# Performance work log

Measured on AMD Instinct MI355X. Metric: run time of the kernel, lower is better.

The kernel has to match this reference:

```python
import jax, jax.numpy as jnp
import numpy as np

FEATURE_SIZE = 40960
FIRST_HIDDEN = 512
HALF = FIRST_HIDDEN // 2  # 256, per-perspective width
SECOND_HIDDEN = 32
BATCH = 4096


def setup_inputs() -> dict:
    key = jax.random.key(0)
    ks = jax.random.split(key, 10)
    inp = {
        "white_features": jax.random.uniform(ks[0], (BATCH, FEATURE_SIZE), dtype=jnp.float32),
        "black_features": jax.random.uniform(ks[1], (BATCH, FEATURE_SIZE), dtype=jnp.float32),
        # input_layer1 and input_layer2 share weight_float/bias_float -> single param
        "w_in": jax.random.normal(ks[2], (HALF, FEATURE_SIZE), dtype=jnp.float32) * 0.1,
        "b_in": jnp.zeros((HALF,), dtype=jnp.float32),
        "w_h1": jax.random.normal(ks[3], (SECOND_HIDDEN, FIRST_HIDDEN), dtype=jnp.float32) * 0.1,
        "b_h1": jnp.zeros((SECOND_HIDDEN,), dtype=jnp.float32),
        "w_h2": jax.random.normal(ks[4], (SECOND_HIDDEN, SECOND_HIDDEN), dtype=jnp.float32) * 0.1,
        "b_h2": jnp.zeros((SECOND_HIDDEN,), dtype=jnp.float32),
        "w_out": jax.random.normal(ks[5], (1, SECOND_HIDDEN), dtype=jnp.float32) * 0.1,
        "b_out": jnp.zeros((1,), dtype=jnp.float32),
    }
    return inp


def _clipped_relu(x):
    return jnp.clip(x, 0.0, 1.0)


def reference(white_features, black_features, w_in, b_in, w_h1, b_h1, w_h2, b_h2, w_out, b_out):
    # Perspective feature transform (shared weights), training-mode float path
    out1 = white_features @ w_in.T + b_in  # [B, 256]
    out2 = black_features @ w_in.T + b_in  # [B, 256]
    x = _clipped_relu(jnp.concatenate([out1, out2], axis=1))  # [B, 512]
    x = _clipped_relu(x @ w_h1.T + b_h1)  # [B, 32]
    x = _clipped_relu(x @ w_h2.T + b_h2)  # [B, 32]
    return x @ w_out.T + b_out  # [B, 1]
```

## Files before the change

### kernel.cpp

```cpp
#include <hip/hip_runtime.h>
#include <hip/hip_fp16.h>


#define FEAT 40960
#define PSTRIDE (8192ull * 256ull)
#define KSPLIT 8
#define KCHUNK (FEAT / KSPLIT)
#define NSTEP 160
#define WTILE_BYTES 16384
#define WWS_BYTES (1280ull * WTILE_BYTES)

using floatx4 = __attribute__((ext_vector_type(4))) float;
using half8   = __attribute__((ext_vector_type(8))) _Float16;

__global__ __launch_bounds__(256) void nnue_wprep(
    const float* __restrict__ w_in, _Float16* __restrict__ Wws)
{
    const int bid = blockIdx.x;
    const int T   = (bid & 7) * NSTEP + (bid >> 3);
    char* base = (char*)Wws + (size_t)T * WTILE_BYTES;
    const int tid = threadIdx.x;
    const int kg0 = T * 32;
#pragma unroll
    for (int i = 0; i < 4; ++i) {
        const int G = tid + i * 256;
        const int r = G >> 2, g = G & 3;
        const float* src = w_in + (size_t)r * FEAT + kg0 + g * 8;
        floatx4 v0 = *reinterpret_cast<const floatx4*>(src);
        floatx4 v1 = *reinterpret_cast<const floatx4*>(src + 4);
        half8 h;
#pragma unroll
        for (int j = 0; j < 4; ++j) { h[j] = (_Float16)v0[j]; h[4 + j] = (_Float16)v1[j]; }
        *reinterpret_cast<half8*>(base + r * 64 + ((g ^ ((r >> 1) & 3)) << 4)) = h;
    }
}

template <typename PT>
__global__ __launch_bounds__(512, 4) void nnue_gemm_v9(
    const float* __restrict__ white, const float* __restrict__ black,
    const _Float16* __restrict__ Wws, PT* __restrict__ P)
{
    __shared__ __align__(16) _Float16 Ws[3][256 * 32];

    const int tid  = threadIdx.x;
    const int lane = tid & 63;
    const int wave = tid >> 6;

    const int ks = blockIdx.x & 7;
    const int mb = blockIdx.x >> 3;

    const float* Abase = (mb < 32)
        ? (white + (size_t)mb * 128 * FEAT)
        : (black + (size_t)(mb - 32) * 128 * FEAT);
    const int k0 = ks * KCHUNK;

    const int frow = lane & 15;
    const int fhi  = lane >> 4;

    const float* Aptr = Abase + (size_t)(wave * 16 + frow) * FEAT + fhi * 8 + k0;

    const int kb = (fhi * 16) ^ (((frow >> 1) & 3) << 4);

    const char* wsrc0 = (const char*)Wws + (size_t)(ks * NSTEP) * WTILE_BYTES
                        + wave * 2048 + lane * 16;

    floatx4 acc[16];
    const floatx4 zero = {0.f, 0.f, 0.f, 0.f};
#pragma unroll
    for (int n = 0; n < 16; ++n) acc[n] = zero;

    floatx4 raA0, raA1, raB0, raB1;

    auto issueW = [&](int t, int wb) {
        const char* g = wsrc0 + (size_t)t * WTILE_BYTES;
        char* l = (char*)&Ws[wb][0] + wave * 2048;
        __builtin_amdgcn_global_load_lds(
            (const __attribute__((address_space(1))) unsigned int*)g,
            (__attribute__((address_space(3))) unsigned int*)l, 16, 0, 0);
        __builtin_amdgcn_global_load_lds(
            (const __attribute__((address_space(1))) unsigned int*)(g + 1024),
            (__attribute__((address_space(3))) unsigned int*)(l + 1024), 16, 0, 0);
    };

    auto cvt = [&](const floatx4& a0, const floatx4& a1) {
        half8 h;
#pragma unroll
        for (int j = 0; j < 4; ++j) { h[j] = (_Float16)a0[j]; h[4 + j] = (_Float16)a1[j]; }
        return h;
    };

    auto mfmaStep = [&](int wb, half8 af) {
        const char* wbase = (const char*)&Ws[wb][0];
#pragma unroll
        for (int n = 0; n < 16; ++n) {
            half8 bf = *reinterpret_cast<const half8*>(
                wbase + (n * 16 + frow) * 64 + kb);
            acc[n] = __builtin_amdgcn_mfma_f32_16x16x32_f16(af, bf, acc[n], 0, 0, 0);
        }
    };

    auto stepf = [&](int t, int wbW, int wbR,
                     floatx4& c0, floatx4& c1, floatx4& n0, floatx4& n1) {
        issueW(t + 2, wbW);
        __builtin_amdgcn_sched_barrier(0);
        n0 = *reinterpret_cast<const floatx4*>(Aptr + (size_t)(t + 1) * 32);
        n1 = *reinterpret_cast<const floatx4*>(Aptr + (size_t)(t + 1) * 32 + 4);
        half8 af = cvt(c0, c1);
        mfmaStep(wbR, af);
        asm volatile("s_waitcnt vmcnt(4) lgkmcnt(0)" ::: "memory");
        __builtin_amdgcn_s_barrier();
        __builtin_amdgcn_sched_barrier(0);
    };

    issueW(0, 0);
    issueW(1, 1);
    __builtin_amdgcn_sched_barrier(0);
    raA0 = *reinterpret_cast<const floatx4*>(Aptr);
    raA1 = *reinterpret_cast<const floatx4*>(Aptr + 4);
    asm volatile("s_waitcnt vmcnt(4)" ::: "memory");
    __builtin_amdgcn_s_barrier();
    __builtin_amdgcn_sched_barrier(0);

    for (int tb = 0; tb < 156; tb += 6) {
        stepf(tb + 0, 2, 0, raA0, raA1, raB0, raB1);
        stepf(tb + 1, 0, 1, raB0, raB1, raA0, raA1);
        stepf(tb + 2, 1, 2, raA0, raA1, raB0, raB1);
        stepf(tb + 3, 2, 0, raB0, raB1, raA0, raA1);
        stepf(tb + 4, 0, 1, raA0, raA1, raB0, raB1);
        stepf(tb + 5, 1, 2, raB0, raB1, raA0, raA1);
    }
    stepf(156, 2, 0, raA0, raA1, raB0, raB1);
    stepf(157, 0, 1, raB0, raB1, raA0, raA1);
    raB0 = *reinterpret_cast<const floatx4*>(Aptr + (size_t)159 * 32);
    raB1 = *reinterpret_cast<const floatx4*>(Aptr + (size_t)159 * 32 + 4);
    {
        half8 af = cvt(raA0, raA1);
        mfmaStep(2, af);
    }
    asm volatile("s_waitcnt vmcnt(4) lgkmcnt(0)" ::: "memory");
    __builtin_amdgcn_s_barrier();
    __builtin_amdgcn_sched_barrier(0);
    {
        half8 af = cvt(raB0, raB1);
        mfmaStep(0, af);
    }

    PT* Pb = P + (size_t)ks * PSTRIDE + (size_t)mb * 128 * 256;
#pragma unroll
    for (int n = 0; n < 16; ++n)
#pragma unroll
        for (int r = 0; r < 4; ++r) {
            const int row = wave * 16 + fhi * 4 + r;
            const int col = n * 16 + frow;
            Pb[(size_t)row * 256 + col] = (PT)acc[n][r];
        }
}

template <typename PT>
__global__ __launch_bounds__(256) void nnue_tail(
    const PT* __restrict__ P,
    const float* __restrict__ b_in,
    const float* __restrict__ w_h1, const float* __restrict__ b_h1,
    const float* __restrict__ w_h2, const float* __restrict__ b_h2,
    const float* __restrict__ w_out, const float* __restrict__ b_out,
    float* __restrict__ out)
{
    __shared__ float xs[32][512];
    __shared__ float w1[32][513];
    __shared__ float w2[32][33];
    __shared__ float h1[32][33];
    __shared__ float h2[32][33];
    __shared__ float wo[32];

    const int tid = threadIdx.x;
    const int b0  = blockIdx.x * 32;

    for (int i = tid; i < 32 * 512; i += 256) w1[i >> 9][i & 511] = w_h1[i];
    for (int i = tid; i < 32 * 32; i += 256)  w2[i >> 5][i & 31]  = w_h2[i];
    if (tid < 32) wo[tid] = w_out[tid];

    for (int i = tid; i < 32 * 512; i += 256) {
        const int r = i >> 9, c = i & 511;
        const int persp = c >> 8, n = c & 255;
        const size_t prow = (size_t)(b0 + r) + (persp ? 4096u : 0u);
        float v = 0.f;
#pragma unroll
        for (int s = 0; s < KSPLIT; ++s)
            v += (float)P[(size_t)s * PSTRIDE + prow * 256 + n];
        v += b_in[n];
        xs[r][c] = fminf(fmaxf(v, 0.f), 1.f);
    }
    __syncthreads();

    for (int p = tid; p < 32 * 32; p += 256) {
        const int o = p & 31, r = p >> 5;
        float a = b_h1[o];
        for (int j = 0; j < 512; ++j) a += xs[r][j] * w1[o][j];
        h1[r][o] = fminf(fmaxf(a, 0.f), 1.f);
    }
    __syncthreads();

    for (int p = tid; p < 32 * 32; p += 256) {
        const int o = p & 31, r = p >> 5;
        float a = b_h2[o];
        for (int j = 0; j < 32; ++j) a += h1[r][j] * w2[o][j];
        h2[r][o] = fminf(fmaxf(a, 0.f), 1.f);
    }
    __syncthreads();

    if (tid < 32) {
        float a = b_out[0];
        for (int j = 0; j < 32; ++j) a += h2[tid][j] * wo[j];
        out[b0 + tid] = a;
    }
}

__global__ __launch_bounds__(256) void nnue_naive(
    const float* __restrict__ white, const float* __restrict__ black,
    const float* __restrict__ w_in, const float* __restrict__ b_in,
    const float* __restrict__ w_h1, const float* __restrict__ b_h1,
    const float* __restrict__ w_h2, const float* __restrict__ b_h2,
    const float* __restrict__ w_out, const float* __restrict__ b_out,
    float* __restrict__ out)
{
    __shared__ float feat[4096];
    __shared__ float xs[512];
    __shared__ float h1s[32];
    __shared__ float h2s[32];
    const int b = blockIdx.x, tid = threadIdx.x;
    float acc0 = 0.f, acc1 = 0.f;
    for (int c = 0; c < FEAT; c += 2048) {
        for (int i = tid; i < 2048; i += 256) {
            feat[i]        = white[(size_t)b * FEAT + c + i];
            feat[2048 + i] = black[(size_t)b * FEAT + c + i];
        }
        __syncthreads();
        const float* wr = w_in + (size_t)tid * FEAT + c;
        for (int k = 0; k < 2048; ++k) {
            const float w = wr[k];
            acc0 += feat[k] * w;
            acc1 += feat[2048 + k] * w;
        }
        __syncthreads();
    }
    xs[tid]       = fminf(fmaxf(acc0 + b_in[tid], 0.f), 1.f);
    xs[256 + tid] = fminf(fmaxf(acc1 + b_in[tid], 0.f), 1.f);
    __syncthreads();
    if (tid < 32) {
        float a = b_h1[tid];
        for (int j = 0; j < 512; ++j) a += xs[j] * w_h1[tid * 512 + j];
        h1s[tid] = fminf(fmaxf(a, 0.f), 1.f);
    }
    __syncthreads();
    if (tid < 32) {
        float a = b_h2[tid];
        for (int j = 0; j < 32; ++j) a += h1s[j] * w_h2[tid * 32 + j];
        h2s[tid] = fminf(fmaxf(a, 0.f), 1.f);
    }
    __syncthreads();
    if (tid == 0) {
        float a = b_out[0];
        for (int j = 0; j < 32; ++j) a += h2s[j] * w_out[j];
        out[b] = a;
    }
}

extern "C" void kernel_launch(void* const* d_in, const int* in_sizes, int n_in,
                              void* d_out, int out_size, void* d_ws, size_t ws_size,
                              hipStream_t stream)
{
    const float* white = (const float*)d_in[0];
    const float* black = (const float*)d_in[1];
    const float* w_in  = (const float*)d_in[2];
    const float* b_in  = (const float*)d_in[3];
    const float* w_h1  = (const float*)d_in[4];
    const float* b_h1  = (const float*)d_in[5];
    const float* w_h2  = (const float*)d_in[6];
    const float* b_h2  = (const float*)d_in[7];
    const float* w_out = (const float*)d_in[8];
    const float* b_out = (const float*)d_in[9];
    float* out = (float*)d_out;

    const size_t pF32 = KSPLIT * PSTRIDE * sizeof(float);
    const size_t pF16 = KSPLIT * PSTRIDE * sizeof(_Float16);

    if (ws_size >= pF32 + WWS_BYTES) {
        float* P = (float*)d_ws;
        _Float16* Wws = (_Float16*)((char*)d_ws + pF32);
        nnue_wprep<<<dim3(1280), 256, 0, stream>>>(w_in, Wws);
        nnue_gemm_v9<float><<<dim3(512), 512, 0, stream>>>(white, black, Wws, P);
        nnue_tail<float><<<dim3(128), 256, 0, stream>>>(P, b_in, w_h1, b_h1,
                                                        w_h2, b_h2, w_out, b_out, out);
    } else if (ws_size >= pF16 + WWS_BYTES) {
        _Float16* P = (_Float16*)d_ws;
        _Float16* Wws = (_Float16*)((char*)d_ws + pF16);
        nnue_wprep<<<dim3(1280), 256, 0, stream>>>(w_in, Wws);
        nnue_gemm_v9<_Float16><<<dim3(512), 512, 0, stream>>>(white, black, Wws, P);
        nnue_tail<_Float16><<<dim3(128), 256, 0, stream>>>(P, b_in, w_h1, b_h1,
                                                           w_h2, b_h2, w_out, b_out, out);
    } else {
        nnue_naive<<<4096, 256, 0, stream>>>(white, black, w_in, b_in, w_h1, b_h1,
                                             w_h2, b_h2, w_out, b_out, out);
    }
}
```

Measured before the change: 393.9 us.

## Process two K-steps per barrier with four LDS weight buffers

New measurement: 390.4 us. About the same (-0.9%).

```diff
diff --git a/kernel.cpp b/kernel.cpp
--- a/kernel.cpp
+++ b/kernel.cpp
@@ -36,11 +36,11 @@
 }
 
 template <typename PT>
-__global__ __launch_bounds__(512, 4) void nnue_gemm_v9(
+__global__ __launch_bounds__(512, 4) void nnue_gemm_v10(
     const float* __restrict__ white, const float* __restrict__ black,
     const _Float16* __restrict__ Wws, PT* __restrict__ P)
 {
-    __shared__ __align__(16) _Float16 Ws[3][256 * 32];
+    __shared__ __align__(16) _Float16 Ws[4][256 * 32];
 
     const int tid  = threadIdx.x;
     const int lane = tid & 63;
@@ -69,7 +69,7 @@
 #pragma unroll
     for (int n = 0; n < 16; ++n) acc[n] = zero;
 
-    floatx4 raA0, raA1, raB0, raB1;
+    floatx4 cA0, cA1, cA2, cA3, nA0, nA1, nA2, nA3;
 
     auto issueW = [&](int t, int wb) {
         const char* g = wsrc0 + (size_t)t * WTILE_BYTES;
@@ -99,14 +99,20 @@
         }
     };
 
-    auto stepf = [&](int t, int wbW, int wbR,
-                     floatx4& c0, floatx4& c1, floatx4& n0, floatx4& n1) {
-        issueW(t + 2, wbW);
+    auto groupf = [&](int g,
+                      floatx4& c0, floatx4& c1, floatx4& c2, floatx4& c3,
+                      floatx4& n0, floatx4& n1, floatx4& n2, floatx4& n3,
+                      int rb0, int rb1, int wb0, int wb1) {
+        const int t0 = 2 * g;
+        issueW(t0 + 2, wb0);
+        issueW(t0 + 3, wb1);
         __builtin_amdgcn_sched_barrier(0);
-        n0 = *reinterpret_cast<const floatx4*>(Aptr + (size_t)(t + 1) * 32);
-        n1 = *reinterpret_cast<const floatx4*>(Aptr + (size_t)(t + 1) * 32 + 4);
-        half8 af = cvt(c0, c1);
-        mfmaStep(wbR, af);
+        n0 = *reinterpret_cast<const floatx4*>(Aptr + (size_t)(t0 + 2) * 32);
+        n1 = *reinterpret_cast<const floatx4*>(Aptr + (size_t)(t0 + 2) * 32 + 4);
+        n2 = *reinterpret_cast<const floatx4*>(Aptr + (size_t)(t0 + 3) * 32);
+        n3 = *reinterpret_cast<const floatx4*>(Aptr + (size_t)(t0 + 3) * 32 + 4);
+        mfmaStep(rb0, cvt(c0, c1));
+        mfmaStep(rb1, cvt(c2, c3));
         asm volatile("s_waitcnt vmcnt(4) lgkmcnt(0)" ::: "memory");
         __builtin_amdgcn_s_barrier();
         __builtin_amdgcn_sched_barrier(0);
@@ -115,35 +121,21 @@
     issueW(0, 0);
     issueW(1, 1);
     __builtin_amdgcn_sched_barrier(0);
-    raA0 = *reinterpret_cast<const floatx4*>(Aptr);
-    raA1 = *reinterpret_cast<const floatx4*>(Aptr + 4);
+    cA0 = *reinterpret_cast<const floatx4*>(Aptr);
+    cA1 = *reinterpret_cast<const floatx4*>(Aptr + 4);
+    cA2 = *reinterpret_cast<const floatx4*>(Aptr + 32);
+    cA3 = *reinterpret_cast<const floatx4*>(Aptr + 32 + 4);
     asm volatile("s_waitcnt vmcnt(4)" ::: "memory");
     __builtin_amdgcn_s_barrier();
     __builtin_amdgcn_sched_barrier(0);
 
-    for (int tb = 0; tb < 156; tb += 6) {
-        stepf(tb + 0, 2, 0, raA0, raA1, raB0, raB1);
-        stepf(tb + 1, 0, 1, raB0, raB1, raA0, raA1);
-        stepf(tb + 2, 1, 2, raA0, raA1, raB0, raB1);
-        stepf(tb + 3, 2, 0, raB0, raB1, raA0, raA1);
-        stepf(tb + 4, 0, 1, raA0, raA1, raB0, raB1);
-        stepf(tb + 5, 1, 2, raB0, raB1, raA0, raA1);
-    }
-    stepf(156, 2, 0, raA0, raA1, raB0, raB1);
-    stepf(157, 0, 1, raB0, raB1, raA0, raA1);
-    raB0 = *reinterpret_cast<const floatx4*>(Aptr + (size_t)159 * 32);
-    raB1 = *reinterpret_cast<const floatx4*>(Aptr + (size_t)159 * 32 + 4);
-    {
-        half8 af = cvt(raA0, raA1);
-        mfmaStep(2, af);
-    }
-    asm volatile("s_waitcnt vmcnt(4) lgkmcnt(0)" ::: "memory");
-    __builtin_amdgcn_s_barrier();
-    __builtin_amdgcn_sched_barrier(0);
-    {
-        half8 af = cvt(raB0, raB1);
-        mfmaStep(0, af);
-    }
+    for (int p = 0; p < 39; ++p) {
+        groupf(2 * p,     cA0, cA1, cA2, cA3, nA0, nA1, nA2, nA3, 0, 1, 2, 3);
+        groupf(2 * p + 1, nA0, nA1, nA2, nA3, cA0, cA1, cA2, cA3, 2, 3, 0, 1);
+    }
+    groupf(78, cA0, cA1, cA2, cA3, nA0, nA1, nA2, nA3, 0, 1, 2, 3);
+    mfmaStep(2, cvt(nA0, nA1));
+    mfmaStep(3, cvt(nA2, nA3));
 
     PT* Pb = P + (size_t)ks * PSTRIDE + (size_t)mb * 128 * 256;
 #pragma unroll
@@ -288,14 +280,14 @@
         float* P = (float*)d_ws;
         _Float16* Wws = (_Float16*)((char*)d_ws + pF32);
         nnue_wprep<<<dim3(1280), 256, 0, stream>>>(w_in, Wws);
-        nnue_gemm_v9<float><<<dim3(512), 512, 0, stream>>>(white, black, Wws, P);
+        nnue_gemm_v10<float><<<dim3(512), 512, 0, stream>>>(white, black, Wws, P);
         nnue_tail<float><<<dim3(128), 256, 0, stream>>>(P, b_in, w_h1, b_h1,
                                                         w_h2, b_h2, w_out, b_out, out);
     } else if (ws_size >= pF16 + WWS_BYTES) {
         _Float16* P = (_Float16*)d_ws;
         _Float16* Wws = (_Float16*)((char*)d_ws + pF16);
         nnue_wprep<<<dim3(1280), 256, 0, stream>>>(w_in, Wws);
-        nnue_gemm_v9<_Float16><<<dim3(512), 512, 0, stream>>>(white, black, Wws, P);
+        nnue_gemm_v10<_Float16><<<dim3(512), 512, 0, stream>>>(white, black, Wws, P);
         nnue_tail<_Float16><<<dim3(128), 256, 0, stream>>>(P, b_in, w_h1, b_h1,
                                                            w_h2, b_h2, w_out, b_out, out);
     } else {
```

## Fuse first-layer GEMM with MLP tail, dropping split-K partial buffer

Applied to the files above, without the earlier changes.

After: 902.5 us. 129% more time.

```diff
diff --git a/kernel.cpp b/kernel.cpp
--- a/kernel.cpp
+++ b/kernel.cpp
@@ -3,12 +3,9 @@
 
 
 #define FEAT 40960
-#define PSTRIDE (8192ull * 256ull)
-#define KSPLIT 8
-#define KCHUNK (FEAT / KSPLIT)
-#define NSTEP 160
+#define NSTEP 1280
 #define WTILE_BYTES 16384
-#define WWS_BYTES (1280ull * WTILE_BYTES)
+#define WWS_BYTES ((size_t)NSTEP * WTILE_BYTES)
 
 using floatx4 = __attribute__((ext_vector_type(4))) float;
 using half8   = __attribute__((ext_vector_type(8))) _Float16;
@@ -16,8 +13,7 @@
 __global__ __launch_bounds__(256) void nnue_wprep(
     const float* __restrict__ w_in, _Float16* __restrict__ Wws)
 {
-    const int bid = blockIdx.x;
-    const int T   = (bid & 7) * NSTEP + (bid >> 3);
+    const int T = blockIdx.x;
     char* base = (char*)Wws + (size_t)T * WTILE_BYTES;
     const int tid = threadIdx.x;
     const int kg0 = T * 32;
@@ -35,45 +31,50 @@
     }
 }
 
-template <typename PT>
-__global__ __launch_bounds__(512, 4) void nnue_gemm_v9(
+__global__ __launch_bounds__(512, 2) void nnue_fused(
     const float* __restrict__ white, const float* __restrict__ black,
-    const _Float16* __restrict__ Wws, PT* __restrict__ P)
-{
-    __shared__ __align__(16) _Float16 Ws[3][256 * 32];
+    const _Float16* __restrict__ Wws,
+    const float* __restrict__ b_in,
+    const float* __restrict__ w_h1, const float* __restrict__ b_h1,
+    const float* __restrict__ w_h2, const float* __restrict__ b_h2,
+    const float* __restrict__ w_out, const float* __restrict__ b_out,
+    float* __restrict__ out)
+{
+    __shared__ __align__(16) _Float16 Ws[8][256 * 32];
+    __shared__ _Float16 xs[16][520];
+    __shared__ float h1s[16][33];
+    __shared__ float h2s[16][33];
 
     const int tid  = threadIdx.x;
     const int lane = tid & 63;
     const int wave = tid >> 6;
-
-    const int ks = blockIdx.x & 7;
-    const int mb = blockIdx.x >> 3;
-
-    const float* Abase = (mb < 32)
-        ? (white + (size_t)mb * 128 * FEAT)
-        : (black + (size_t)(mb - 32) * 128 * FEAT);
-    const int k0 = ks * KCHUNK;
+    const int ws   = wave >> 2;
+    const int wn   = wave & 3;
+
+    const int b0 = blockIdx.x * 16;
 
     const int frow = lane & 15;
     const int fhi  = lane >> 4;
 
-    const float* Aptr = Abase + (size_t)(wave * 16 + frow) * FEAT + fhi * 8 + k0;
+    const float* Abase = (ws ? black : white) + (size_t)(b0 + frow) * FEAT + fhi * 8;
 
     const int kb = (fhi * 16) ^ (((frow >> 1) & 3) << 4);
 
-    const char* wsrc0 = (const char*)Wws + (size_t)(ks * NSTEP) * WTILE_BYTES
-                        + wave * 2048 + lane * 16;
-
-    floatx4 acc[16];
+    const char* wsrc0 = (const char*)Wws + wave * 2048 + lane * 16;
+
+    const int t0 = (blockIdx.x * 5) % 128;
+    auto wrap = [](int x) { return (x >= NSTEP) ? x - NSTEP : x; };
+
+    floatx4 acc[4];
     const floatx4 zero = {0.f, 0.f, 0.f, 0.f};
 #pragma unroll
-    for (int n = 0; n < 16; ++n) acc[n] = zero;
-
-    floatx4 raA0, raA1, raB0, raB1;
-
-    auto issueW = [&](int t, int wb) {
+    for (int n = 0; n < 4; ++n) acc[n] = zero;
+
+    floatx4 cA[8], nA[8];
+
+    auto issueW = [&](int t, int buf) {
         const char* g = wsrc0 + (size_t)t * WTILE_BYTES;
-        char* l = (char*)&Ws[wb][0] + wave * 2048;
+        char* l = (char*)&Ws[buf][0] + wave * 2048;
         __builtin_amdgcn_global_load_lds(
             (const __attribute__((address_space(1))) unsigned int*)g,
             (__attribute__((address_space(3))) unsigned int*)l, 16, 0, 0);
@@ -82,6 +83,21 @@
             (__attribute__((address_space(3))) unsigned int*)(l + 1024), 16, 0, 0);
     };
 
+    auto issueW4 = [&](int p0, int p1, int p2, int p3, int bb) {
+        issueW(p0, bb); issueW(p1, bb + 1); issueW(p2, bb + 2); issueW(p3, bb + 3);
+    };
+
+    auto loadA4 = [&](floatx4 (&ra)[8], int p0, int p1, int p2, int p3) {
+        ra[0] = *reinterpret_cast<const floatx4*>(Abase + (size_t)p0 * 32);
+        ra[1] = *reinterpret_cast<const floatx4*>(Abase + (size_t)p0 * 32 + 4);
+        ra[2] = *reinterpret_cast<const floatx4*>(Abase + (size_t)p1 * 32);
+        ra[3] = *reinterpret_cast<const floatx4*>(Abase + (size_t)p1 * 32 + 4);
+        ra[4] = *reinterpret_cast<const floatx4*>(Abase + (size_t)p2 * 32);
+        ra[5] = *reinterpret_cast<const floatx4*>(Abase + (size_t)p2 * 32 + 4);
+        ra[6] = *reinterpret_cast<const floatx4*>(Abase + (size_t)p3 * 32);
+        ra[7] = *reinterpret_cast<const floatx4*>(Abase + (size_t)p3 * 32 + 4);
+    };
+
     auto cvt = [&](const floatx4& a0, const floatx4& a1) {
         half8 h;
 #pragma unroll
@@ -89,128 +105,90 @@
         return h;
     };
 
-    auto mfmaStep = [&](int wb, half8 af) {
-        const char* wbase = (const char*)&Ws[wb][0];
-#pragma unroll
-        for (int n = 0; n < 16; ++n) {
-            half8 bf = *reinterpret_cast<const half8*>(
-                wbase + (n * 16 + frow) * 64 + kb);
-            acc[n] = __builtin_amdgcn_mfma_f32_16x16x32_f16(af, bf, acc[n], 0, 0, 0);
-        }
-    };
-
-    auto stepf = [&](int t, int wbW, int wbR,
-                     floatx4& c0, floatx4& c1, floatx4& n0, floatx4& n1) {
-        issueW(t + 2, wbW);
-        __builtin_amdgcn_sched_barrier(0);
-        n0 = *reinterpret_cast<const floatx4*>(Aptr + (size_t)(t + 1) * 32);
-        n1 = *reinterpret_cast<const floatx4*>(Aptr + (size_t)(t + 1) * 32 + 4);
-        half8 af = cvt(c0, c1);
-        mfmaStep(wbR, af);
-        asm volatile("s_waitcnt vmcnt(4) lgkmcnt(0)" ::: "memory");
+    auto mfma4 = [&](int bb, floatx4 (&ra)[8]) {
+#pragma unroll
+        for (int s = 0; s < 4; ++s) {
+            half8 af = cvt(ra[2 * s], ra[2 * s + 1]);
+            const char* wbase = (const char*)&Ws[bb + s][0];
+#pragma unroll
+            for (int n = 0; n < 4; ++n) {
+                const int r = wn * 64 + n * 16 + frow;
+                half8 bf = *reinterpret_cast<const half8*>(wbase + r * 64 + kb);
+                acc[n] = __builtin_amdgcn_mfma_f32_16x16x32_f16(af, bf, acc[n], 0, 0, 0);
+            }
+        }
+    };
+
+    auto grp = [&](int p0, int p1, int p2, int p3,
+                   floatx4 (&cc)[8], floatx4 (&nn)[8], int rb, int wb) {
+        issueW4(p0, p1, p2, p3, wb);
+        __builtin_amdgcn_sched_barrier(0);
+        loadA4(nn, p0, p1, p2, p3);
+        mfma4(rb, cc);
+        asm volatile("s_waitcnt vmcnt(8) lgkmcnt(0)" ::: "memory");
         __builtin_amdgcn_s_barrier();
         __builtin_amdgcn_sched_barrier(0);
     };
 
-    issueW(0, 0);
-    issueW(1, 1);
-    __builtin_amdgcn_sched_barrier(0);
-    raA0 = *reinterpret_cast<const floatx4*>(Aptr);
-    raA1 = *reinterpret_cast<const floatx4*>(Aptr + 4);
-    asm volatile("s_waitcnt vmcnt(4)" ::: "memory");
+    {
+        const int p0 = t0, p1 = wrap(t0 + 1), p2 = wrap(t0 + 2), p3 = wrap(t0 + 3);
+        issueW4(p0, p1, p2, p3, 0);
+        __builtin_amdgcn_sched_barrier(0);
+        loadA4(cA, p0, p1, p2, p3);
+        asm volatile("s_waitcnt vmcnt(8)" ::: "memory");
+        __builtin_amdgcn_s_barrier();
+        __builtin_amdgcn_sched_barrier(0);
+    }
+
+    for (int p = 0; p < 159; ++p) {
+        const int i0 = 8 * p;
+        grp(wrap(t0 + i0 + 4), wrap(t0 + i0 + 5), wrap(t0 + i0 + 6), wrap(t0 + i0 + 7),
+            cA, nA, 0, 4);
+        grp(wrap(t0 + i0 + 8), wrap(t0 + i0 + 9), wrap(t0 + i0 + 10), wrap(t0 + i0 + 11),
+            nA, cA, 4, 0);
+    }
+    grp(wrap(t0 + 1276), wrap(t0 + 1277), wrap(t0 + 1278), wrap(t0 + 1279),
+        cA, nA, 0, 4);
+    mfma4(4, nA);
+    asm volatile("s_waitcnt vmcnt(0) lgkmcnt(0)" ::: "memory");
     __builtin_amdgcn_s_barrier();
     __builtin_amdgcn_sched_barrier(0);
 
-    for (int tb = 0; tb < 156; tb += 6) {
-        stepf(tb + 0, 2, 0, raA0, raA1, raB0, raB1);
-        stepf(tb + 1, 0, 1, raB0, raB1, raA0, raA1);
-        stepf(tb + 2, 1, 2, raA0, raA1, raB0, raB1);
-        stepf(tb + 3, 2, 0, raB0, raB1, raA0, raA1);
-        stepf(tb + 4, 0, 1, raA0, raA1, raB0, raB1);
-        stepf(tb + 5, 1, 2, raB0, raB1, raA0, raA1);
-    }
-    stepf(156, 2, 0, raA0, raA1, raB0, raB1);
-    stepf(157, 0, 1, raB0, raB1, raA0, raA1);
-    raB0 = *reinterpret_cast<const floatx4*>(Aptr + (size_t)159 * 32);
-    raB1 = *reinterpret_cast<const floatx4*>(Aptr + (size_t)159 * 32 + 4);
+#pragma unroll
+    for (int n = 0; n < 4; ++n) {
+        const int bcol = wn * 64 + n * 16 + frow;
+        const float bi = b_in[bcol];
+#pragma unroll
+        for (int r = 0; r < 4; ++r) {
+            const int row = fhi * 4 + r;
+            xs[row][ws * 256 + bcol] = (_Float16)fminf(fmaxf(acc[n][r] + bi, 0.f), 1.f);
+        }
+    }
+    __syncthreads();
+
     {
-        half8 af = cvt(raA0, raA1);
-        mfmaStep(2, af);
-    }
-    asm volatile("s_waitcnt vmcnt(4) lgkmcnt(0)" ::: "memory");
-    __builtin_amdgcn_s_barrier();
-    __builtin_amdgcn_sched_barrier(0);
+        const int r = tid >> 5, o = tid & 31;
+        float a = b_h1[o];
+        const float* wrow = w_h1 + o * 512;
+#pragma unroll 8
+        for (int j = 0; j < 512; ++j) a += (float)xs[r][j] * wrow[j];
+        h1s[r][o] = fminf(fmaxf(a, 0.f), 1.f);
+    }
+    __syncthreads();
+
     {
-        half8 af = cvt(raB0, raB1);
-        mfmaStep(0, af);
-    }
-
-    PT* Pb = P + (size_t)ks * PSTRIDE + (size_t)mb * 128 * 256;
-#pragma unroll
-    for (int n = 0; n < 16; ++n)
-#pragma unroll
-        for (int r = 0; r < 4; ++r) {
-            const int row = wave * 16 + fhi * 4 + r;
-            const int col = n * 16 + frow;
-            Pb[(size_t)row * 256 + col] = (PT)acc[n][r];
-        }
-}
-
-template <typename PT>
-__global__ __launch_bounds__(256) void nnue_tail(
-    const PT* __restrict__ P,
-    const float* __restrict__ b_in,
-    const float* __restrict__ w_h1, const float* __restrict__ b_h1,
-    const float* __restrict__ w_h2, const float* __restrict__ b_h2,
-    const float* __restrict__ w_out, const float* __restrict__ b_out,
-    float* __restrict__ out)
-{
-    __shared__ float xs[32][512];
-    __shared__ float w1[32][513];
-    __shared__ float w2[32][33];
-    __shared__ float h1[32][33];
-    __shared__ float h2[32][33];
-    __shared__ float wo[32];
-
-    const int tid = threadIdx.x;
-    const int b0  = blockIdx.x * 32;
-
-    for (int i = tid; i < 32 * 512; i += 256) w1[i >> 9][i & 511] = w_h1[i];
-    for (int i = tid; i < 32 * 32; i += 256)  w2[i >> 5][i & 31]  = w_h2[i];
-    if (tid < 32) wo[tid] = w_out[tid];
-
-    for (int i = tid; i < 32 * 512; i += 256) {
-        const int r = i >> 9, c = i & 511;
-        const int persp = c >> 8, n = c & 255;
-        const size_t prow = (size_t)(b0 + r) + (persp ? 4096u : 0u);
-        float v = 0.f;
-#pragma unroll
-        for (int s = 0; s < KSPLIT; ++s)
-            v += (float)P[(size_t)s * PSTRIDE + prow * 256 + n];
-        v += b_in[n];
-        xs[r][c] = fminf(fmaxf(v, 0.f), 1.f);
-    }
-    __syncthreads();
-
-    for (int p = tid; p < 32 * 32; p += 256) {
-        const int o = p & 31, r = p >> 5;
-        float a = b_h1[o];
-        for (int j = 0; j < 512; ++j) a += xs[r][j] * w1[o][j];
-        h1[r][o] = fminf(fmaxf(a, 0.f), 1.f);
-    }
-    __syncthreads();
-
-    for (int p = tid; p < 32 * 32; p += 256) {
-        const int o = p & 31, r = p >> 5;
+        const int r = tid >> 5, o = tid & 31;
         float a = b_h2[o];
-        for (int j = 0; j < 32; ++j) a += h1[r][j] * w2[o][j];
-        h2[r][o] = fminf(fmaxf(a, 0.f), 1.f);
-    }
-    __syncthreads();
-
-    if (tid < 32) {
+#pragma unroll
+        for (int j = 0; j < 32; ++j) a += h1s[r][j] * w_h2[o * 32 + j];
+        h2s[r][o] = fminf(fmaxf(a, 0.f), 1.f);
+    }
+    __syncthreads();
+
+    if (tid < 16) {
         float a = b_out[0];
-        for (int j = 0; j < 32; ++j) a += h2[tid][j] * wo[j];
+#pragma unroll
+        for (int j = 0; j < 32; ++j) a += h2s[tid][j] * w_out[j];
         out[b0 + tid] = a;
     }
 }
@@ -224,7 +202,7 @@
     float* __restrict__ out)
 {
     __shared__ float feat[4096];
-    __shared__ float xs[512];
+    __shared__ float xsv[512];
     __shared__ float h1s[32];
     __shared__ float h2s[32];
     const int b = blockIdx.x, tid = threadIdx.x;
@@ -243,12 +221,12 @@
         }
         __syncthreads();
     }
-    xs[tid]       = fminf(fmaxf(acc0 + b_in[tid], 0.f), 1.f);
-    xs[256 + tid] = fminf(fmaxf(acc1 + b_in[tid], 0.f), 1.f);
+    xsv[tid]       = fminf(fmaxf(acc0 + b_in[tid], 0.f), 1.f);
+    xsv[256 + tid] = fminf(fmaxf(acc1 + b_in[tid], 0.f), 1.f);
     __syncthreads();
     if (tid < 32) {
         float a = b_h1[tid];
-        for (int j = 0; j < 512; ++j) a += xs[j] * w_h1[tid * 512 + j];
+        for (int j = 0; j < 512; ++j) a += xsv[j] * w_h1[tid * 512 + j];
         h1s[tid] = fminf(fmaxf(a, 0.f), 1.f);
     }
     __syncthreads();
@@ -281,23 +259,12 @@
     const float* b_out = (const float*)d_in[9];
     float* out = (float*)d_out;
 
-    const size_t pF32 = KSPLIT * PSTRIDE * sizeof(float);
-    const size_t pF16 = KSPLIT * PSTRIDE * sizeof(_Float16);
-
-    if (ws_size >= pF32 + WWS_BYTES) {
-        float* P = (float*)d_ws;
-        _Float16* Wws = (_Float16*)((char*)d_ws + pF32);
-        nnue_wprep<<<dim3(1280), 256, 0, stream>>>(w_in, Wws);
-        nnue_gemm_v9<float><<<dim3(512), 512, 0, stream>>>(white, black, Wws, P);
-        nnue_tail<float><<<dim3(128), 256, 0, stream>>>(P, b_in, w_h1, b_h1,
-                                                        w_h2, b_h2, w_out, b_out, out);
-    } else if (ws_size >= pF16 + WWS_BYTES) {
-        _Float16* P = (_Float16*)d_ws;
-        _Float16* Wws = (_Float16*)((char*)d_ws + pF16);
-        nnue_wprep<<<dim3(1280), 256, 0, stream>>>(w_in, Wws);
-        nnue_gemm_v9<_Float16><<<dim3(512), 512, 0, stream>>>(white, black, Wws, P);
-        nnue_tail<_Float16><<<dim3(128), 256, 0, stream>>>(P, b_in, w_h1, b_h1,
-                                                           w_h2, b_h2, w_out, b_out, out);
+    if (ws_size >= WWS_BYTES) {
+        _Float16* Wws = (_Float16*)d_ws;
+        nnue_wprep<<<dim3(NSTEP), 256, 0, stream>>>(w_in, Wws);
+        nnue_fused<<<dim3(256), 512, 0, stream>>>(white, black, Wws, b_in,
+                                                  w_h1, b_h1, w_h2, b_h2,
+                                                  w_out, b_out, out);
     } else {
         nnue_naive<<<4096, 256, 0, stream>>>(white, black, w_in, b_in, w_h1, b_h1,
                                              w_h2, b_h2, w_out, b_out, out);
```
